# Optimization experiments

Hardware: AMD Instinct MI355X
Metric: run time of the kernel (lower is better)

Reference implementation:

```python
import jax, jax.numpy as jnp
import numpy as np

# Per-species MLP dims from CoefficientLayer._create_model (H, C, N, O), aev_dim=384
DIMS = {"h": [384, 160, 128, 96, 1], "c": [384, 144, 112, 96, 1], "n": [384, 128, 112, 96, 1], "o": [384, 128, 112, 96, 1]}


def setup_inputs() -> dict:
    key = jax.random.key(0)
    B, A, D = 256, 256, 384
    ks = jax.random.split(key, 64)
    inp = {}
    inp["species"] = jax.random.randint(ks[0], (B, A), 0, 4)  # species index 0..3
    inp["aev"] = jax.random.normal(ks[1], (B, A, D), dtype=jnp.float32)
    inp["b0"] = jnp.array([0.1, 0.2, 0.3, 0.4], dtype=jnp.float32)  # shifter intercepts
    inp["b1"] = jnp.array([1.0, 1.1, 0.9, 1.2], dtype=jnp.float32)  # shifter slopes
    ki = 2
    for name, dims in DIMS.items():
        for l in range(4):
            fi, fo = dims[l], dims[l + 1]
            inp[f"{name}w{l}"] = jax.random.normal(ks[ki], (fi, fo), dtype=jnp.float32) / np.float32(np.sqrt(fi))
            ki += 1
            inp[f"{name}b{l}"] = jnp.zeros((fo,), dtype=jnp.float32)
    return inp


def _mlp(x, ws, bs):
    # Linear -> CELU(0.1) x3 -> Linear(->1), squeeze last dim
    for i in range(3):
        x = jax.nn.celu(x @ ws[i] + bs[i], alpha=0.1)
    return (x @ ws[3] + bs[3])[..., 0]


def reference(species, aev, b0, b1,
              hw0, hb0, hw1, hb1, hw2, hb2, hw3, hb3,
              cw0, cb0, cw1, cb1, cw2, cb2, cw3, cb3,
              nw0, nb0, nw1, nb1, nw2, nb2, nw3, nb3,
              ow0, ob0, ow1, ob1, ow2, ob2, ow3, ob3):
    nets = [
        ([hw0, hw1, hw2, hw3], [hb0, hb1, hb2, hb3]),
        ([cw0, cw1, cw2, cw3], [cb0, cb1, cb2, cb3]),
        ([nw0, nw1, nw2, nw3], [nb0, nb1, nb2, nb3]),
        ([ow0, ow1, ow2, ow3], [ob0, ob1, ob2, ob3]),
    ]
    # ANIModel hard routing: each atom's coefficient comes from its species' network;
    # atoms with species == -1 (padding) stay 0.
    coef = jnp.zeros(species.shape, dtype=aev.dtype)
    for i, (ws, bs) in enumerate(nets):  # fixed small loop over 4 species
        coef = jnp.where(species == i, _mlp(aev, ws, bs), coef)
    # Shifter: result[mask_i] = b0[i] + b1[i] * coef[mask_i]; padding stays 0
    idx = jnp.clip(species, 0)
    return jnp.where(species >= 0, b0[idx] + b1[idx] * coef, jnp.zeros((), dtype=aev.dtype))
```

## Files before the change

### kernel.cpp

```cpp
#include <hip/hip_runtime.h>

typedef _Float16 f16;
typedef _Float16 f16x8 __attribute__((ext_vector_type(8)));
typedef float f32x4 __attribute__((ext_vector_type(4)));
typedef unsigned short u16;

#define NATOMS 65536

#define WS_LISTS_OFF 256
#define WS_W_OFF 524544
#define WS_W_ELEMS 350208
#define WS_NEEDED (WS_W_OFF + WS_W_ELEMS * 2)

struct ConvJob { const float* src; int K, N, KS, NT, off; };

struct PrepParams {
  const int* species;
  int* counts;
  u16* lists;
  f16* wbase;
  ConvJob jobs[16];
};

struct MlpParams {
  const float* aev;
  const float* b0;
  const float* b1;
  const float* bias[4][4];
  const f16* w[4][4];
  const int* counts;
  const u16* lists;
  float* out;
  int Nreal0[4];
  int Nreal1[4];
};

__global__ __launch_bounds__(256) void prep_kernel(PrepParams p) {
  int tid = threadIdx.x;
  if (blockIdx.x < 256) {
    __shared__ int wcnt[4][4];
    __shared__ int wbase[4][4];
    int i = blockIdx.x * 256 + tid;
    int s = p.species[i];
    int wave = tid >> 6, lane = tid & 63;
    unsigned long long m[4];
    #pragma unroll
    for (int t = 0; t < 4; t++) {
      m[t] = __ballot(s == t);
      if (lane == 0) wcnt[wave][t] = __popcll(m[t]);
    }
    __syncthreads();
    if (tid < 4) {
      int t = tid;
      int c0 = wcnt[0][t], c1 = wcnt[1][t], c2 = wcnt[2][t], c3 = wcnt[3][t];
      int base = atomicAdd(&p.counts[t], c0 + c1 + c2 + c3);
      wbase[0][t] = base;
      wbase[1][t] = base + c0;
      wbase[2][t] = base + c0 + c1;
      wbase[3][t] = base + c0 + c1 + c2;
    }
    __syncthreads();
    int rnk = __popcll(m[s] & ((1ull << lane) - 1ull));
    p.lists[s * NATOMS + wbase[wave][s] + rnk] = (u16)i;
  } else {
    int bx = blockIdx.x - 256;
    int job = bx / 30, bxin = bx - job * 30;
    ConvJob jb = p.jobs[job];
    int fid = bxin * 256 + tid;
    int nfrag = jb.KS * jb.NT * 64;
    if (fid >= nfrag) return;
    int ks64 = jb.KS * 64;
    int nt = fid / ks64;
    int rem = fid - nt * ks64;
    int ks = rem >> 6, lane = rem & 63;
    int q = lane >> 4, nlo = lane & 15;
    int n = nt * 16 + nlo;
    int k0 = ks * 32 + q * 8;
    f16x8 v;
    #pragma unroll
    for (int j = 0; j < 8; j++) {
      int k = k0 + j;
      float x = (n < jb.N && k < jb.K) ? jb.src[k * jb.N + n] : 0.f;
      v[j] = (f16)x;
    }
    *(f16x8*)(p.wbase + jb.off + (size_t)fid * 8) = v;
  }
}

__device__ __forceinline__ float celu01(float v) {
  return v > 0.f ? v : 0.1f * (__expf(v * 10.f) - 1.f);
}

__device__ __forceinline__ void stage_frag(const f16* g, f16* l, int lane) {
  __builtin_amdgcn_global_load_lds(
      (const __attribute__((address_space(1))) unsigned int*)(g + lane * 8),
      (__attribute__((address_space(3))) unsigned int*)l, 16, 0, 0);
}

template <int KS, int NT, bool ACT>
__device__ __forceinline__ int layer_lds(const f16x8* a, const f16* __restrict__ Wt,
                                         const float* __restrict__ bias, int Nreal,
                                         f16* dstw, int DS, f16* ring, int r0,
                                         int w, int lane, int q, int nlo) {
  constexpr int SUBS = (KS + 3) / 4;
  constexpr int C = NT * SUBS;
  {
    constexpr int nks0 = (KS < 4) ? KS : 4;
    if (w < nks0)
      stage_frag(Wt + (size_t)w * 512,
                 ring + (size_t)(r0 % 3) * 2048 + w * 512, lane);
  }
  f32x4 acc = {0.f, 0.f, 0.f, 0.f};
  #pragma unroll
  for (int c = 0; c < C; c++) {
    if (c + 1 < C) {
      int nt1 = (c + 1) / SUBS, sub1 = (c + 1) % SUBS;
      int k01 = sub1 * 4;
      int nks1 = (KS - k01 < 4) ? (KS - k01) : 4;
      if (w < nks1)
        stage_frag(Wt + (size_t)(nt1 * KS + k01 + w) * 512,
                   ring + (size_t)((r0 + c + 1) % 3) * 2048 + w * 512, lane);
    }
    __syncthreads();
    int nt = c / SUBS, sub = c % SUBS;
    int k0 = sub * 4;
    int nks = (KS - k0 < 4) ? (KS - k0) : 4;
    const f16* slot = ring + (size_t)((r0 + c) % 3) * 2048;
    if (sub == 0) acc = f32x4{0.f, 0.f, 0.f, 0.f};
    #pragma unroll
    for (int j = 0; j < 4; j++) {
      if (j < nks) {
        f16x8 b = *(const f16x8*)(slot + (j * 64 + lane) * 8);
        acc = __builtin_amdgcn_mfma_f32_16x16x32_f16(a[k0 + j], b, acc, 0, 0, 0);
      }
    }
    if (sub == SUBS - 1) {
      int n = nt * 16 + nlo;
      float bv = (n < Nreal) ? bias[n] : 0.f;
      #pragma unroll
      for (int r = 0; r < 4; r++) {
        float v = acc[r] + bv;
        if (ACT) v = celu01(v);
        dstw[(q * 4 + r) * DS + n] = (f16)v;
      }
    }
  }
  return (r0 + C) % 3;
}

template <int NT0, int KS1>
__device__ __forceinline__ void mlp_body(const MlpParams& p, int s, int tile,
                                         f16* ring, f16* Bf0, f16* Bf1) {
  int cnt = p.counts[s];
  if (tile * 64 >= cnt) return;
  const u16* list = p.lists + s * NATOMS;
  int tid = threadIdx.x, w = tid >> 6, lane = tid & 63;
  int q = lane >> 4, nlo = lane & 15;
  int rowbase = tile * 64 + w * 16;

  int rr = rowbase + nlo;
  int atom = list[min(rr, cnt - 1)];

  f16x8 a0[12];
  const float* ap = p.aev + (size_t)atom * 384 + q * 8;
  #pragma unroll
  for (int ks = 0; ks < 12; ks++) {
    float4 u0 = *(const float4*)(ap + ks * 32);
    float4 u1 = *(const float4*)(ap + ks * 32 + 4);
    f16x8 t = {(f16)u0.x, (f16)u0.y, (f16)u0.z, (f16)u0.w,
               (f16)u1.x, (f16)u1.y, (f16)u1.z, (f16)u1.w};
    a0[ks] = t;
  }

  f16* my0 = Bf0 + (w * 16) * 168;
  f16* my1 = Bf1 + (w * 16) * 136;

  int r0 = 0;
  r0 = layer_lds<12, NT0, true>(a0, p.w[s][0], p.bias[s][0], p.Nreal0[s],
                                my0, 168, ring, r0, w, lane, q, nlo);

  f16x8 a1[KS1];
  #pragma unroll
  for (int ks = 0; ks < KS1; ks++)
    a1[ks] = *(const f16x8*)(my0 + nlo * 168 + ks * 32 + q * 8);
  r0 = layer_lds<KS1, 8, true>(a1, p.w[s][1], p.bias[s][1], p.Nreal1[s],
                               my1, 136, ring, r0, w, lane, q, nlo);

  f16x8 a2[4];
  #pragma unroll
  for (int ks = 0; ks < 4; ks++)
    a2[ks] = *(const f16x8*)(my1 + nlo * 136 + ks * 32 + q * 8);
  r0 = layer_lds<4, 6, true>(a2, p.w[s][2], p.bias[s][2], 96,
                             my0, 168, ring, r0, w, lane, q, nlo);

  f16x8 a3[3];
  #pragma unroll
  for (int ks = 0; ks < 3; ks++)
    a3[ks] = *(const f16x8*)(my0 + nlo * 168 + ks * 32 + q * 8);
  f32x4 acc = {0.f, 0.f, 0.f, 0.f};
  const f16* W3 = p.w[s][3];
  #pragma unroll
  for (int ks = 0; ks < 3; ks++) {
    f16x8 b = *(const f16x8*)(W3 + (size_t)(ks * 64 + lane) * 8);
    acc = __builtin_amdgcn_mfma_f32_16x16x32_f16(a3[ks], b, acc, 0, 0, 0);
  }
  if (nlo == 0) {
    float b3 = p.bias[s][3][0];
    float b0v = p.b0[s], b1v = p.b1[s];
    #pragma unroll
    for (int r = 0; r < 4; r++) {
      int m = rowbase + q * 4 + r;
      if (m < cnt) {
        float coef = acc[r] + b3;
        p.out[list[m]] = b0v + b1v * coef;
      }
    }
  }
}

__global__ __launch_bounds__(256, 3) void mlp_kernel(MlpParams p) {
  __shared__ f16 ring[3 * 2048];
  __shared__ f16 Bf0[64 * 168];
  __shared__ f16 Bf1[64 * 136];
  int s = blockIdx.x & 3;
  int tile = blockIdx.x >> 2;
  switch (s) {
    case 0: mlp_body<10, 5>(p, 0, tile, ring, Bf0, Bf1); break;
    case 1: mlp_body<10, 5>(p, 1, tile, ring, Bf0, Bf1); break;
    case 2: mlp_body<8, 4>(p, 2, tile, ring, Bf0, Bf1); break;
    default: mlp_body<8, 4>(p, 3, tile, ring, Bf0, Bf1); break;
  }
}

extern "C" void kernel_launch(void* const* d_in, const int* in_sizes, int n_in,
                              void* d_out, int out_size, void* d_ws, size_t ws_size,
                              hipStream_t stream) {
  if (ws_size < WS_NEEDED) return;

  const int* species = (const int*)d_in[0];
  const float* aev = (const float*)d_in[1];
  const float* b0 = (const float*)d_in[2];
  const float* b1 = (const float*)d_in[3];

  static const int F1[4]  = {160, 144, 128, 128};
  static const int F1p[4] = {160, 160, 128, 128};
  static const int F2[4]  = {128, 112, 112, 112};

  char* wsb = (char*)d_ws;
  int* counts = (int*)wsb;
  u16* lists = (u16*)(wsb + WS_LISTS_OFF);
  f16* wbase = (f16*)(wsb + WS_W_OFF);

  PrepParams pp;
  pp.species = species; pp.counts = counts; pp.lists = lists; pp.wbase = wbase;

  MlpParams mp;
  mp.aev = aev; mp.b0 = b0; mp.b1 = b1;
  mp.counts = counts; mp.lists = lists; mp.out = (float*)d_out;

  int off = 0, ji = 0;
  for (int s = 0; s < 4; s++) {
    int K[4]  = {384, F1[s], F2[s], 96};
    int N[4]  = {F1[s], F2[s], 96, 1};
    int KS[4] = {12, F1p[s] / 32, 4, 3};
    int NT[4] = {F1p[s] / 16, 8, 6, 1};
    for (int l = 0; l < 4; l++) {
      const float* w = (const float*)d_in[4 + s * 8 + l * 2];
      const float* b = (const float*)d_in[4 + s * 8 + l * 2 + 1];
      pp.jobs[ji].src = w;
      pp.jobs[ji].K = K[l];
      pp.jobs[ji].N = N[l];
      pp.jobs[ji].KS = KS[l];
      pp.jobs[ji].NT = NT[l];
      pp.jobs[ji].off = off;
      mp.w[s][l] = wbase + off;
      mp.bias[s][l] = b;
      off += KS[l] * NT[l] * 512;
      ji++;
    }
    mp.Nreal0[s] = F1[s];
    mp.Nreal1[s] = F2[s];
  }

  hipMemsetAsync(d_ws, 0, 64, stream);
  prep_kernel<<<dim3(256 + 480), 256, 0, stream>>>(pp);
  mlp_kernel<<<dim3(280 * 4), 256, 0, stream>>>(mp);
}
```

Measured before the change: 264.5 us.

## Restructure MLP layers into K-chunked double-buffered weight staging across all N tiles

The weight layout in the prep kernel is reordered into K-chunks of two k-steps spanning all N tiles. Each layer now stages a whole chunk into a two-slot LDS ring and keeps one accumulator per N tile. The first chunk of the next layer's weights is prefetched during the last chunk of the current layer, so the per-layer pipeline restart goes away. This cuts the number of barriers per layer and lets many independent MFMAs run between syncs. The cost is a larger LDS ring and more accumulator registers, so launch bounds drop from 3 to 2 blocks per SM.

```diff
diff --git a/kernel.cpp b/kernel.cpp
--- a/kernel.cpp
+++ b/kernel.cpp
@@ -6,13 +6,14 @@
 typedef unsigned short u16;
 
 #define NATOMS 65536
+#define SLOT 10240
 
 #define WS_LISTS_OFF 256
 #define WS_W_OFF 524544
 #define WS_W_ELEMS 350208
 #define WS_NEEDED (WS_W_OFF + WS_W_ELEMS * 2)
 
-struct ConvJob { const float* src; int K, N, KS, NT, off; };
+struct ConvJob { const float* src; int K, N, KS, NT, CK, off; };
 
 struct PrepParams {
   const int* species;
@@ -66,13 +67,15 @@
     int bx = blockIdx.x - 256;
     int job = bx / 30, bxin = bx - job * 30;
     ConvJob jb = p.jobs[job];
-    int fid = bxin * 256 + tid;
-    int nfrag = jb.KS * jb.NT * 64;
-    if (fid >= nfrag) return;
-    int ks64 = jb.KS * 64;
-    int nt = fid / ks64;
-    int rem = fid - nt * ks64;
-    int ks = rem >> 6, lane = rem & 63;
+    int e = bxin * 256 + tid;
+    int nslots = jb.KS * jb.NT * 64;
+    if (e >= nslots) return;
+    int frag = e >> 6, lane = e & 63;
+    int c = frag / (jb.CK * jb.NT);
+    int rem = frag - c * (jb.CK * jb.NT);
+    int ckc = min(jb.CK, jb.KS - c * jb.CK);
+    int nt = rem / ckc, ki = rem - nt * ckc;
+    int ks = c * jb.CK + ki;
     int q = lane >> 4, nlo = lane & 15;
     int n = nt * 16 + nlo;
     int k0 = ks * 32 + q * 8;
@@ -83,7 +86,7 @@
       float x = (n < jb.N && k < jb.K) ? jb.src[k * jb.N + n] : 0.f;
       v[j] = (f16)x;
     }
-    *(f16x8*)(p.wbase + jb.off + (size_t)fid * 8) = v;
+    *(f16x8*)(p.wbase + jb.off + (size_t)e * 8) = v;
   }
 }
 
@@ -97,55 +100,53 @@
       (__attribute__((address_space(3))) unsigned int*)l, 16, 0, 0);
 }
 
-template <int KS, int NT, bool ACT>
-__device__ __forceinline__ int layer_lds(const f16x8* a, const f16* __restrict__ Wt,
+template <int KS, int NT, int CK>
+__device__ __forceinline__ int run_layer(const f16x8* a, const f16* __restrict__ Wt,
                                          const float* __restrict__ bias, int Nreal,
-                                         f16* dstw, int DS, f16* ring, int r0,
-                                         int w, int lane, int q, int nlo) {
-  constexpr int SUBS = (KS + 3) / 4;
-  constexpr int C = NT * SUBS;
-  {
-    constexpr int nks0 = (KS < 4) ? KS : 4;
-    if (w < nks0)
-      stage_frag(Wt + (size_t)w * 512,
-                 ring + (size_t)(r0 % 3) * 2048 + w * 512, lane);
-  }
-  f32x4 acc = {0.f, 0.f, 0.f, 0.f};
+                                         f16* dstw, int DS, f16* ring, int par,
+                                         const f16* nextW, int nextNF,
+                                         f32x4* acc, int w, int lane, int q, int nlo) {
+  constexpr int C = (KS + CK - 1) / CK;
+  #pragma unroll
+  for (int nt = 0; nt < NT; nt++) acc[nt] = f32x4{0.f, 0.f, 0.f, 0.f};
   #pragma unroll
   for (int c = 0; c < C; c++) {
+    f16* cur = ring + par * SLOT;
+    f16* nxt = ring + (par ^ 1) * SLOT;
     if (c + 1 < C) {
-      int nt1 = (c + 1) / SUBS, sub1 = (c + 1) % SUBS;
-      int k01 = sub1 * 4;
-      int nks1 = (KS - k01 < 4) ? (KS - k01) : 4;
-      if (w < nks1)
-        stage_frag(Wt + (size_t)(nt1 * KS + k01 + w) * 512,
-                   ring + (size_t)((r0 + c + 1) % 3) * 2048 + w * 512, lane);
+      const f16* gb = Wt + (size_t)((c + 1) * CK * NT) * 512;
+      int nf = min(CK, KS - (c + 1) * CK) * NT;
+      for (int f = w; f < nf; f += 4)
+        stage_frag(gb + (size_t)f * 512, nxt + f * 512, lane);
+    } else if (nextNF > 0) {
+      for (int f = w; f < nextNF; f += 4)
+        stage_frag(nextW + (size_t)f * 512, nxt + f * 512, lane);
+    }
+    int ckc = min(CK, KS - c * CK);
+    #pragma unroll
+    for (int nt = 0; nt < NT; nt++) {
+      #pragma unroll
+      for (int ki = 0; ki < CK; ki++) {
+        if (ki < ckc) {
+          f16x8 b = *(const f16x8*)(cur + (nt * ckc + ki) * 512 + lane * 8);
+          acc[nt] = __builtin_amdgcn_mfma_f32_16x16x32_f16(a[c * CK + ki], b, acc[nt], 0, 0, 0);
+        }
+      }
     }
     __syncthreads();
-    int nt = c / SUBS, sub = c % SUBS;
-    int k0 = sub * 4;
-    int nks = (KS - k0 < 4) ? (KS - k0) : 4;
-    const f16* slot = ring + (size_t)((r0 + c) % 3) * 2048;
-    if (sub == 0) acc = f32x4{0.f, 0.f, 0.f, 0.f};
-    #pragma unroll
-    for (int j = 0; j < 4; j++) {
-      if (j < nks) {
-        f16x8 b = *(const f16x8*)(slot + (j * 64 + lane) * 8);
-        acc = __builtin_amdgcn_mfma_f32_16x16x32_f16(a[k0 + j], b, acc, 0, 0, 0);
-      }
-    }
-    if (sub == SUBS - 1) {
-      int n = nt * 16 + nlo;
-      float bv = (n < Nreal) ? bias[n] : 0.f;
-      #pragma unroll
-      for (int r = 0; r < 4; r++) {
-        float v = acc[r] + bv;
-        if (ACT) v = celu01(v);
-        dstw[(q * 4 + r) * DS + n] = (f16)v;
-      }
-    }
-  }
-  return (r0 + C) % 3;
+    par ^= 1;
+  }
+  #pragma unroll
+  for (int nt = 0; nt < NT; nt++) {
+    int n = nt * 16 + nlo;
+    float bv = (n < Nreal) ? bias[n] : 0.f;
+    #pragma unroll
+    for (int r = 0; r < 4; r++) {
+      float v = celu01(acc[nt][r] + bv);
+      dstw[(q * 4 + r) * DS + n] = (f16)v;
+    }
+  }
+  return par;
 }
 
 template <int NT0, int KS1>
@@ -157,9 +158,7 @@
   int tid = threadIdx.x, w = tid >> 6, lane = tid & 63;
   int q = lane >> 4, nlo = lane & 15;
   int rowbase = tile * 64 + w * 16;
-
-  int rr = rowbase + nlo;
-  int atom = list[min(rr, cnt - 1)];
+  int atom = list[min(rowbase + nlo, cnt - 1)];
 
   f16x8 a0[12];
   const float* ap = p.aev + (size_t)atom * 384 + q * 8;
@@ -172,37 +171,42 @@
     a0[ks] = t;
   }
 
+  for (int f = w; f < 2 * NT0; f += 4)
+    stage_frag(p.w[s][0] + (size_t)f * 512, ring + f * 512, lane);
+  __syncthreads();
+
   f16* my0 = Bf0 + (w * 16) * 168;
   f16* my1 = Bf1 + (w * 16) * 136;
-
-  int r0 = 0;
-  r0 = layer_lds<12, NT0, true>(a0, p.w[s][0], p.bias[s][0], p.Nreal0[s],
-                                my0, 168, ring, r0, w, lane, q, nlo);
+  f32x4 acc[10];
+
+  int par = 0;
+  par = run_layer<12, NT0, 2>(a0, p.w[s][0], p.bias[s][0], p.Nreal0[s], my0, 168,
+                              ring, par, p.w[s][1], 16, acc, w, lane, q, nlo);
 
   f16x8 a1[KS1];
   #pragma unroll
   for (int ks = 0; ks < KS1; ks++)
     a1[ks] = *(const f16x8*)(my0 + nlo * 168 + ks * 32 + q * 8);
-  r0 = layer_lds<KS1, 8, true>(a1, p.w[s][1], p.bias[s][1], p.Nreal1[s],
-                               my1, 136, ring, r0, w, lane, q, nlo);
+  par = run_layer<KS1, 8, 2>(a1, p.w[s][1], p.bias[s][1], p.Nreal1[s], my1, 136,
+                             ring, par, p.w[s][2], 12, acc, w, lane, q, nlo);
 
   f16x8 a2[4];
   #pragma unroll
   for (int ks = 0; ks < 4; ks++)
     a2[ks] = *(const f16x8*)(my1 + nlo * 136 + ks * 32 + q * 8);
-  r0 = layer_lds<4, 6, true>(a2, p.w[s][2], p.bias[s][2], 96,
-                             my0, 168, ring, r0, w, lane, q, nlo);
+  par = run_layer<4, 6, 2>(a2, p.w[s][2], p.bias[s][2], 96, my0, 168,
+                           ring, par, (const f16*)0, 0, acc, w, lane, q, nlo);
 
   f16x8 a3[3];
   #pragma unroll
   for (int ks = 0; ks < 3; ks++)
     a3[ks] = *(const f16x8*)(my0 + nlo * 168 + ks * 32 + q * 8);
-  f32x4 acc = {0.f, 0.f, 0.f, 0.f};
+  f32x4 acc3 = {0.f, 0.f, 0.f, 0.f};
   const f16* W3 = p.w[s][3];
   #pragma unroll
   for (int ks = 0; ks < 3; ks++) {
     f16x8 b = *(const f16x8*)(W3 + (size_t)(ks * 64 + lane) * 8);
-    acc = __builtin_amdgcn_mfma_f32_16x16x32_f16(a3[ks], b, acc, 0, 0, 0);
+    acc3 = __builtin_amdgcn_mfma_f32_16x16x32_f16(a3[ks], b, acc3, 0, 0, 0);
   }
   if (nlo == 0) {
     float b3 = p.bias[s][3][0];
@@ -211,15 +215,15 @@
     for (int r = 0; r < 4; r++) {
       int m = rowbase + q * 4 + r;
       if (m < cnt) {
-        float coef = acc[r] + b3;
+        float coef = acc3[r] + b3;
         p.out[list[m]] = b0v + b1v * coef;
       }
     }
   }
 }
 
-__global__ __launch_bounds__(256, 3) void mlp_kernel(MlpParams p) {
-  __shared__ f16 ring[3 * 2048];
+__global__ __launch_bounds__(256, 2) void mlp_kernel(MlpParams p) {
+  __shared__ f16 ring[2 * SLOT];
   __shared__ f16 Bf0[64 * 168];
   __shared__ f16 Bf1[64 * 136];
   int s = blockIdx.x & 3;
@@ -264,6 +268,7 @@
     int N[4]  = {F1[s], F2[s], 96, 1};
     int KS[4] = {12, F1p[s] / 32, 4, 3};
     int NT[4] = {F1p[s] / 16, 8, 6, 1};
+    int CK[4] = {2, 2, 2, 3};
     for (int l = 0; l < 4; l++) {
       const float* w = (const float*)d_in[4 + s * 8 + l * 2];
       const float* b = (const float*)d_in[4 + s * 8 + l * 2 + 1];
@@ -272,6 +277,7 @@
       pp.jobs[ji].N = N[l];
       pp.jobs[ji].KS = KS[l];
       pp.jobs[ji].NT = NT[l];
+      pp.jobs[ji].CK = CK[l];
       pp.jobs[ji].off = off;
       mp.w[s][l] = wbase + off;
       mp.bias[s][l] = b;
```

Result: slower. 284.1 us (+7.4%).
